# Performance work log

Measured on AMD Instinct MI355X. Metric: run time of the kernel, lower is better.

Reference implementation:

```python
import jax, jax.numpy as jnp
import numpy as np

BATCH = 1_048_576  # number of mesh vertices (2x2 metric tensors)


def _sym2x2(v):
    """[B,3] -> [B,2,2] symmetric matrix [[a,b],[b,c]], matching torch.stack layout."""
    a, b, c = v[:, 0], v[:, 1], v[:, 2]
    row0 = jnp.stack([a, b], axis=-1)
    row1 = jnp.stack([b, c], axis=-1)
    return jnp.stack([row0, row1], axis=-2)


def matrix_operator(A, operator):
    """Faithful port: eigh, apply op to eigenvalues, reconstruct with inv(V)."""
    w, V = jnp.linalg.eigh(A)
    if operator == 'exp':
        w = jnp.exp(w)
    elif operator == 'log':
        w = jnp.log(w)
    else:
        w = jnp.power(w, operator)
    # V @ diag(w) @ inv(V); scale columns of V by w to avoid diag_embed
    return (V * w[..., None, :]) @ jnp.linalg.inv(V)


def setup_inputs() -> dict:
    key = jax.random.key(0)
    k1, k2 = jax.random.split(key)
    prediction = 0.5 * jax.random.normal(k1, (BATCH, 3), dtype=jnp.float32)
    # actual must encode SPD 2x2 matrices: M = L L^T + 0.1 I
    L = 0.5 * jax.random.normal(k2, (BATCH, 2, 2), dtype=jnp.float32)
    M = L @ jnp.swapaxes(L, -1, -2) + 0.1 * jnp.eye(2, dtype=jnp.float32)
    actual = jnp.stack([M[:, 0, 0], M[:, 0, 1], M[:, 1, 1]], axis=-1)
    return {"prediction": prediction, "actual": actual}


def reference(prediction, actual):
    S_0 = _sym2x2(prediction)            # [B,2,2] predicted log-metric
    M = _sym2x2(actual)                  # [B,2,2] SPD target metric
    M_0 = matrix_operator(S_0, 'exp')    # exp(S_0), SPD
    M_0_temp = jnp.linalg.inv(matrix_operator(M_0, 0.5))  # M_0^{-1/2}
    transformed_M = M_0_temp @ M @ M_0_temp
    S = matrix_operator(transformed_M, 'log')
    frobenius_norm_squared = jnp.sum(S ** 2, axis=(-2, -1))  # [B]
    return jnp.mean(frobenius_norm_squared)
```

## Files before the change

kernel.cpp:

```cpp
#include <hip/hip_runtime.h>
#include <math.h>

#define NPART 1024
#define BLOCK 256

__device__ __forceinline__ float block_reduce_sum(float v) {
    __shared__ float smem[BLOCK / 64];
    const int lane = threadIdx.x & 63;
    const int wave = threadIdx.x >> 6;
    #pragma unroll
    for (int off = 32; off > 0; off >>= 1)
        v += __shfl_down(v, off, 64);
    if (lane == 0) smem[wave] = v;
    __syncthreads();
    if (wave == 0) {
        v = (lane < (BLOCK / 64)) ? smem[lane] : 0.0f;
        v += __shfl_down(v, 2, 64);
        v += __shfl_down(v, 1, 64);
    }
    return v;
}

__device__ __forceinline__ float metric_elem(float p0, float p1, float p2,
                                             float m00, float m01, float m11) {
    const float am = -0.25f * (p0 + p2);
    const float ad = -0.25f * (p0 - p2);
    const float ab = -0.5f  * p1;
    const float ar = sqrtf(ad * ad + ab * ab);
    const float e1 = __expf(am + ar);
    const float e2 = __expf(am - ar);
    const float ec0 = 0.5f * (e1 + e2);
    const float ec1 = 0.5f * (e1 - e2) / fmaxf(ar, 1e-20f);
    const float t00 = ec0 + ec1 * ad;
    const float t01 = ec1 * ab;
    const float t11 = ec0 - ec1 * ad;

    const float x00 = t00 * m00 + t01 * m01;
    const float x01 = t00 * m01 + t01 * m11;
    const float x10 = t01 * m00 + t11 * m01;
    const float x11 = t01 * m01 + t11 * m11;
    const float r00 = x00 * t00 + x01 * t01;
    const float r01 = x00 * t01 + x01 * t11;
    const float r10 = x10 * t00 + x11 * t01;
    const float r11 = x10 * t01 + x11 * t11;
    const float rb  = 0.5f * (r01 + r10);

    const float lm = 0.5f * (r00 + r11);
    const float ld = 0.5f * (r00 - r11);
    const float lr = sqrtf(ld * ld + rb * rb);
    const float lam1 = lm + lr;
    const float lam2 = fmaxf(lm - lr, 1e-30f);
    const float g1 = __logf(lam1);
    const float g2 = __logf(lam2);
    const float lc0 = 0.5f * (g1 + g2);
    const float lc1 = 0.5f * (g1 - g2) / fmaxf(lr, 1e-20f);
    const float s00 = lc0 + lc1 * ld;
    const float s01 = lc1 * rb;
    const float s11 = lc0 - lc1 * ld;

    return s00 * s00 + s11 * s11 + 2.0f * s01 * s01;
}

__global__ __launch_bounds__(BLOCK) void metric_partial_kernel(
        const float* __restrict__ pred, const float* __restrict__ act,
        float* __restrict__ partial, int B) {
    const int tid = blockIdx.x * BLOCK + threadIdx.x;
    const int stride = gridDim.x * BLOCK;
    const int G = B >> 2;
    const float4* __restrict__ p4 = (const float4*)pred;
    const float4* __restrict__ a4 = (const float4*)act;

    float acc = 0.0f;
    for (int g = tid; g < G; g += stride) {
        const float4 pa = p4[3 * g + 0];
        const float4 pb = p4[3 * g + 1];
        const float4 pc = p4[3 * g + 2];
        const float4 qa = a4[3 * g + 0];
        const float4 qb = a4[3 * g + 1];
        const float4 qc = a4[3 * g + 2];
        acc += metric_elem(pa.x, pa.y, pa.z, qa.x, qa.y, qa.z);
        acc += metric_elem(pa.w, pb.x, pb.y, qa.w, qb.x, qb.y);
        acc += metric_elem(pb.z, pb.w, pc.x, qb.z, qb.w, qc.x);
        acc += metric_elem(pc.y, pc.z, pc.w, qc.y, qc.z, qc.w);
    }
    const int tail_start = G << 2;
    for (int i = tail_start + tid; i < B; i += stride) {
        acc += metric_elem(pred[3 * i], pred[3 * i + 1], pred[3 * i + 2],
                           act[3 * i], act[3 * i + 1], act[3 * i + 2]);
    }

    const float bsum = block_reduce_sum(acc);
    if (threadIdx.x == 0) partial[blockIdx.x] = bsum;
}

__global__ __launch_bounds__(BLOCK) void metric_final_kernel(
        const float* __restrict__ partial, float* __restrict__ out,
        int n, float inv_b) {
    float acc = 0.0f;
    for (int i = threadIdx.x; i < n; i += BLOCK) acc += partial[i];
    const float total = block_reduce_sum(acc);
    if (threadIdx.x == 0) out[0] = total * inv_b;
}

extern "C" void kernel_launch(void* const* d_in, const int* in_sizes, int n_in,
                              void* d_out, int out_size, void* d_ws, size_t ws_size,
                              hipStream_t stream) {
    const float* pred = (const float*)d_in[0];
    const float* act  = (const float*)d_in[1];
    float* out = (float*)d_out;
    float* partial = (float*)d_ws;

    const int B = in_sizes[0] / 3;

    metric_partial_kernel<<<NPART, BLOCK, 0, stream>>>(pred, act, partial, B);
    metric_final_kernel<<<1, BLOCK, 0, stream>>>(partial, out, NPART, 1.0f / (float)B);
}
```

Measured before the change: 12.89 us.

## Compute log-metric norm from eigenvalues via trace and determinant

```diff
diff --git a/kernel.cpp b/kernel.cpp
--- a/kernel.cpp
+++ b/kernel.cpp
@@ -23,42 +23,25 @@
 
 __device__ __forceinline__ float metric_elem(float p0, float p1, float p2,
                                              float m00, float m01, float m11) {
-    const float am = -0.25f * (p0 + p2);
-    const float ad = -0.25f * (p0 - p2);
-    const float ab = -0.5f  * p1;
-    const float ar = sqrtf(ad * ad + ab * ab);
-    const float e1 = __expf(am + ar);
-    const float e2 = __expf(am - ar);
-    const float ec0 = 0.5f * (e1 + e2);
-    const float ec1 = 0.5f * (e1 - e2) / fmaxf(ar, 1e-20f);
-    const float t00 = ec0 + ec1 * ad;
-    const float t01 = ec1 * ab;
-    const float t11 = ec0 - ec1 * ad;
+    const float am = -0.5f * (p0 + p2);
+    const float ad = -0.5f * (p0 - p2);
+    const float ab = -p1;
+    const float r  = sqrtf(ad * ad + ab * ab);
+    const float e1 = __expf(am + r);
+    const float e2 = __expf(am - r);
+    const float c0 = 0.5f * (e1 + e2);
+    const float c1 = 0.5f * (e1 - e2) / fmaxf(r, 1e-20f);
 
-    const float x00 = t00 * m00 + t01 * m01;
-    const float x01 = t00 * m01 + t01 * m11;
-    const float x10 = t01 * m00 + t11 * m01;
-    const float x11 = t01 * m01 + t11 * m11;
-    const float r00 = x00 * t00 + x01 * t01;
-    const float r01 = x00 * t01 + x01 * t11;
-    const float r10 = x10 * t00 + x11 * t01;
-    const float r11 = x10 * t01 + x11 * t11;
-    const float rb  = 0.5f * (r01 + r10);
+    const float trR  = c0 * (m00 + m11) + c1 * (ad * (m00 - m11) + 2.0f * ab * m01);
+    const float detR = (e1 * e2) * (m00 * m11 - m01 * m01);
 
-    const float lm = 0.5f * (r00 + r11);
-    const float ld = 0.5f * (r00 - r11);
-    const float lr = sqrtf(ld * ld + rb * rb);
-    const float lam1 = lm + lr;
-    const float lam2 = fmaxf(lm - lr, 1e-30f);
-    const float g1 = __logf(lam1);
-    const float g2 = __logf(lam2);
-    const float lc0 = 0.5f * (g1 + g2);
-    const float lc1 = 0.5f * (g1 - g2) / fmaxf(lr, 1e-20f);
-    const float s00 = lc0 + lc1 * ld;
-    const float s01 = lc1 * rb;
-    const float s11 = lc0 - lc1 * ld;
+    const float h  = 0.5f * trR;
+    const float q  = sqrtf(fmaxf(h * h - detR, 0.0f));
+    const float mu1 = h + q;
 
-    return s00 * s00 + s11 * s11 + 2.0f * s01 * s01;
+    const float g1 = __logf(mu1);
+    const float g2 = __logf(detR) - g1;
+    return g1 * g1 + g2 * g2;
 }
 
 __global__ __launch_bounds__(BLOCK) void metric_partial_kernel(
```

New measurement: 12.38 us. -4.0%, faster.
